# Optimization experiments

Measured on AMD Instinct MI355X. Metric: run time of the kernel, lower is better.

## Reference

```python
import jax, jax.numpy as jnp
import numpy as np

NUM_HEADS = 12
NEG_INF = -1e30  # stand-in for -inf; exp underflows to 0 identically, avoids nan in grads


def setup_inputs() -> dict:
    key = jax.random.key(0)
    ks = jax.random.split(key, 8)
    B, H, W, EXTRA, C = 8, 32, 32, 64, 768
    N = H * W + EXTRA  # 1088 image tokens + task tokens
    hd = C // NUM_HEADS  # 64
    s = 0.02
    x = jax.random.normal(ks[0], (B, N, C), dtype=jnp.float32)
    qkv_w = jax.random.normal(ks[1], (3 * C, C), dtype=jnp.float32) * s
    qkv_b = jax.random.normal(ks[2], (3 * C,), dtype=jnp.float32) * s
    proj_w = jax.random.normal(ks[3], (C, C), dtype=jnp.float32) * s
    proj_b = jax.random.normal(ks[4], (C,), dtype=jnp.float32) * s
    rel_pos_h = jax.random.normal(ks[5], (2 * H - 1, hd), dtype=jnp.float32) * s
    rel_pos_w = jax.random.normal(ks[6], (2 * W - 1, hd), dtype=jnp.float32) * s
    # mask the trailing 32 key tokens per batch element (rows keep valid keys)
    key_padding_mask = jnp.broadcast_to(jnp.arange(N)[None, :] >= N - 32, (B, N))
    return {"x": x, "qkv_w": qkv_w, "qkv_b": qkv_b, "proj_w": proj_w,
            "proj_b": proj_b, "rel_pos_h": rel_pos_h, "rel_pos_w": rel_pos_w,
            "key_padding_mask": key_padding_mask, "H": H, "W": W}


def _get_rel_pos(q_size, k_size, rel_pos):
    # q_size == k_size and rel_pos.shape[0] == 2*q_size-1 here -> no interpolation branch
    coords = jnp.arange(q_size)[:, None] - jnp.arange(k_size)[None, :] + (k_size - 1)
    return rel_pos[coords]  # (q_size, k_size, head_dim)


def reference(x, qkv_w, qkv_b, proj_w, proj_b, rel_pos_h, rel_pos_w,
              key_padding_mask, H, W):
    B, N, C = x.shape
    nh = NUM_HEADS
    hd = C // nh
    scale = hd ** -0.5
    HW = H * W
    # qkv projection -> (3, B*nh, N, hd)
    qkv = (x @ qkv_w.T + qkv_b).reshape(B, N, 3, nh, hd)
    qkv = jnp.transpose(qkv, (2, 0, 3, 1, 4)).reshape(3, B * nh, N, hd)
    q, k, v = qkv[0], qkv[1], qkv[2]
    attn = jnp.einsum('bqd,bkd->bqk', q * scale, k)  # (B*nh, N, N)
    # decomposed relative position bias on the HxW grid block
    Rh = _get_rel_pos(H, H, rel_pos_h)  # (H, H, hd)
    Rw = _get_rel_pos(W, W, rel_pos_w)  # (W, W, hd)
    r_q = q[:, :HW].reshape(B * nh, H, W, hd)
    rel_h = jnp.einsum('bhwc,hkc->bhwk', r_q, Rh)  # (B*nh, H, W, H)
    rel_w = jnp.einsum('bhwc,wkc->bhwk', r_q, Rw)  # (B*nh, H, W, W)
    bias = (rel_h[:, :, :, :, None] + rel_w[:, :, :, None, :]).reshape(B * nh, HW, HW)
    attn = attn.at[:, :HW, :HW].add(bias)
    # key padding mask fusion: (B, N) -> (B*nh, 1, N), broadcast over queries
    mask = jnp.broadcast_to(key_padding_mask[:, None, None, :], (B, nh, 1, N))
    mask = mask.reshape(B * nh, 1, N)
    attn = jnp.where(mask, NEG_INF, attn)
    attn = jax.nn.softmax(attn, axis=-1)
    out = jnp.einsum('bqk,bkd->bqd', attn, v).reshape(B, nh, N, hd)
    out = jnp.transpose(out, (0, 2, 1, 3)).reshape(B, N, C)
    return out @ proj_w.T + proj_b
```

## Files before the change

### kernel.cpp

```cpp
#include <hip/hip_runtime.h>
#include <stdint.h>


typedef __attribute__((ext_vector_type(8))) short bf16x8;
typedef __attribute__((ext_vector_type(4))) float f32x4;
typedef __attribute__((ext_vector_type(16))) float f32x16;
typedef __attribute__((ext_vector_type(2))) int i32x2;
typedef __attribute__((ext_vector_type(4))) int i32x4;

#define DEVINL static __device__ __forceinline__

DEVINL unsigned short f2bf(float f) {
  unsigned u = __builtin_bit_cast(unsigned, f);
  u += 0x7FFFu + ((u >> 16) & 1u);
  return (unsigned short)(u >> 16);
}
DEVINL float bf2f(unsigned short h) {
  unsigned u = ((unsigned)h) << 16;
  return __builtin_bit_cast(float, u);
}
DEVINL void gload_lds16(const void* g, void* l) {
  __builtin_amdgcn_global_load_lds(
      (const __attribute__((address_space(1))) unsigned int*)g,
      (__attribute__((address_space(3))) unsigned int*)l, 16, 0, 0);
}
DEVINL float exp2_hw(float x) {
  float r;
  asm("v_exp_f32 %0, %1" : "=v"(r) : "v"(x));
  return r;
}
DEVINL unsigned cvtpk_bf16(float lo, float hi) {
  unsigned r;
  asm("v_cvt_pk_bf16_f32 %0, %1, %2" : "=v"(r) : "v"(lo), "v"(hi));
  return r;
}

__global__ void k_cvt(const float* __restrict__ in, unsigned short* __restrict__ out, int n4) {
  int i = blockIdx.x * 256 + threadIdx.x;
  int stride = gridDim.x * 256;
  for (; i < n4; i += stride) {
    float4 v = ((const float4*)in)[i];
    ushort4 o = make_ushort4(f2bf(v.x), f2bf(v.y), f2bf(v.z), f2bf(v.w));
    ((ushort4*)out)[i] = o;
  }
}

__global__ void k_cvt2(const float* __restrict__ a, const float* __restrict__ b,
                       unsigned short* __restrict__ oa, unsigned short* __restrict__ ob,
                       int n4each) {
  int i = blockIdx.x * 256 + threadIdx.x;
  if (i < n4each) {
    float4 v = ((const float4*)a)[i];
    ((ushort4*)oa)[i] = make_ushort4(f2bf(v.x), f2bf(v.y), f2bf(v.z), f2bf(v.w));
  } else if (i < 2 * n4each) {
    int j = i - n4each;
    float4 v = ((const float4*)b)[j];
    ((ushort4*)ob)[j] = make_ushort4(f2bf(v.x), f2bf(v.y), f2bf(v.z), f2bf(v.w));
  }
}

template <int EPI, int NT, int JPX>
__global__ __launch_bounds__(256) void k_gemm_bt(
    const unsigned short* __restrict__ A, const unsigned short* __restrict__ Bm,
    const float* __restrict__ bias, float* __restrict__ Cf,
    unsigned short* __restrict__ oq, unsigned short* __restrict__ ok,
    unsigned short* __restrict__ ov, int M, int N, int K) {
  __shared__ __align__(16) unsigned short lA[128 * 64];
  __shared__ __align__(16) unsigned short lB[128 * 64];
  const int f = blockIdx.y * gridDim.x + blockIdx.x;
  const int job = (f & 7) * JPX + (f >> 3);
  const int xt = job / NT, yt = job - xt * NT;
  const int t = threadIdx.x;
  const int w = t >> 6, l = t & 63;
  const int wm = w >> 1, wn = w & 1;
  const int g = l >> 4, li = l & 15;
  const int row0 = xt * 128, col0 = yt * 128;
  const unsigned short* Ab = A + (size_t)row0 * K;
  const unsigned short* Bb = Bm + (size_t)col0 * K;
  const f32x4 zero = {0.f, 0.f, 0.f, 0.f};
  f32x4 acc[4][4];
#pragma unroll
  for (int i = 0; i < 4; ++i)
#pragma unroll
    for (int j = 0; j < 4; ++j) acc[i][j] = zero;

  const int srow = t >> 3;
  const int scs = (t & 7) ^ (srow & 7);

  for (int kt = 0; kt < K; kt += 64) {
#pragma unroll
    for (int p = 0; p < 4; ++p) {
      int r = p * 32 + srow;
      gload_lds16(Ab + (size_t)r * K + kt + scs * 8, lA + p * 2048 + w * 512);
      gload_lds16(Bb + (size_t)r * K + kt + scs * 8, lB + p * 2048 + w * 512);
    }
    __syncthreads();
#pragma unroll
    for (int kh = 0; kh < 2; ++kh) {
      bf16x8 af[4], bfv[4];
#pragma unroll
      for (int mf = 0; mf < 4; ++mf) {
        int r = wm * 64 + mf * 16 + li;
        int c8 = (kh * 4 + g) ^ (r & 7);
        af[mf] = *(const bf16x8*)(lA + r * 64 + c8 * 8);
      }
#pragma unroll
      for (int nf = 0; nf < 4; ++nf) {
        int r = wn * 64 + nf * 16 + li;
        int c8 = (kh * 4 + g) ^ (r & 7);
        bfv[nf] = *(const bf16x8*)(lB + r * 64 + c8 * 8);
      }
#pragma unroll
      for (int mf = 0; mf < 4; ++mf)
#pragma unroll
        for (int nf = 0; nf < 4; ++nf)
          acc[mf][nf] = __builtin_amdgcn_mfma_f32_16x16x32_bf16(af[mf], bfv[nf], acc[mf][nf], 0, 0, 0);
    }
    __syncthreads();
  }

#pragma unroll
  for (int mf = 0; mf < 4; ++mf) {
#pragma unroll
    for (int nf = 0; nf < 4; ++nf) {
      const int jc = col0 + wn * 64 + nf * 16 + li;
      const float bj = bias[jc];
#pragma unroll
      for (int rg = 0; rg < 4; ++rg) {
        const int m = row0 + wm * 64 + mf * 16 + g * 4 + rg;
        float val = acc[mf][nf][rg] + bj;
        if (EPI == 0) {
          int which = jc / 768;
          int jr = jc - which * 768;
          int head = jr >> 6, d = jr & 63;
          int b = m / 1088;
          int n = m - b * 1088;
          size_t idx = (((size_t)(b * 12 + head)) * 1088 + n) * 64 + d;
          if (which == 0) val *= 0.18033688011112042f;
          unsigned short bv = f2bf(val);
          if (which == 0) oq[idx] = bv;
          else if (which == 1) ok[idx] = bv;
          else ov[idx] = bv;
        } else {
          Cf[(size_t)m * N + jc] = val;
        }
      }
    }
  }
}

__global__ __launch_bounds__(256) void k_vt(const unsigned short* __restrict__ v,
                                            unsigned short* __restrict__ vt) {
  __shared__ unsigned short tile[64 * 66];
  const int bh = blockIdx.y, nt = blockIdx.x, t = threadIdx.x;
  const unsigned short* src = v + (((size_t)bh * 1088) + nt * 64) * 64;
#pragma unroll
  for (int i = 0; i < 2; ++i) {
    int c = t + 256 * i;
    int r = c >> 3, d8 = (c & 7) * 8;
    uint4 val = *(const uint4*)(src + (size_t)r * 64 + d8);
    const unsigned short* s8 = (const unsigned short*)&val;
#pragma unroll
    for (int j = 0; j < 8; ++j) tile[r * 66 + d8 + j] = s8[j];
  }
  __syncthreads();
  unsigned short* dst = vt + ((size_t)bh * 64) * 1088 + nt * 64;
#pragma unroll
  for (int i = 0; i < 2; ++i) {
    int c = t + 256 * i;
    int d = c >> 3, n8 = (c & 7) * 8;
    unsigned short tmp[8];
#pragma unroll
    for (int j = 0; j < 8; ++j) tmp[j] = tile[(n8 + j) * 66 + d];
    *(uint4*)(dst + (size_t)d * 1088 + n8) = *(const uint4*)tmp;
  }
}

__global__ __launch_bounds__(256) void k_relpos(const unsigned short* __restrict__ qbf,
                                                const unsigned short* __restrict__ rphbf,
                                                const unsigned short* __restrict__ rpwbf,
                                                float* __restrict__ relhT,
                                                float* __restrict__ relw) {
  __shared__ float gw[4][32 * 64];
  const int bh = blockIdx.y, t = threadIdx.x;
  const int wv = t >> 6, l = t & 63;
  const int h = blockIdx.x * 4 + wv;
  const int lk = l & 31, hf = l >> 5;

  bf16x8 qf[4];
  {
    const unsigned short* qp = qbf + (((size_t)bh * 1088) + h * 32 + lk) * 64 + hf * 8;
#pragma unroll
    for (int db = 0; db < 4; ++db) qf[db] = *(const bf16x8*)(qp + db * 16);
  }

  f32x16 dh, g0, g1;
#pragma unroll
  for (int i = 0; i < 16; ++i) { dh[i] = 0.f; g0[i] = 0.f; g1[i] = 0.f; }

  {
    const unsigned short* bp = rphbf + (size_t)(h + 31 - lk) * 64 + hf * 8;
#pragma unroll
    for (int db = 0; db < 4; ++db) {
      bf16x8 bfr = *(const bf16x8*)(bp + db * 16);
      dh = __builtin_amdgcn_mfma_f32_32x32x16_bf16(qf[db], bfr, dh, 0, 0, 0);
    }
  }
  {
    const unsigned short* bp0 = rpwbf + (size_t)lk * 64 + hf * 8;
    const unsigned short* bp1 = rpwbf + (size_t)(32 + lk) * 64 + hf * 8;
#pragma unroll
    for (int db = 0; db < 4; ++db) {
      bf16x8 b0 = *(const bf16x8*)(bp0 + db * 16);
      bf16x8 b1 = *(const bf16x8*)(bp1 + db * 16);
      g0 = __builtin_amdgcn_mfma_f32_32x32x16_bf16(qf[db], b0, g0, 0, 0, 0);
      g1 = __builtin_amdgcn_mfma_f32_32x32x16_bf16(qf[db], b1, g1, 0, 0, 0);
    }
  }
  float* G = gw[wv];
#pragma unroll
  for (int i = 0; i < 16; ++i) {
    int row = (i & 3) + 8 * (i >> 2) + 4 * hf;
    G[row * 64 + lk] = g0[i];
    G[row * 64 + 32 + lk] = g1[i];
  }
  f32x16 dwv;
#pragma unroll
  for (int i = 0; i < 16; ++i) {
    int row = (i & 3) + 8 * (i >> 2) + 4 * hf;
    dwv[i] = G[row * 65 + 31 - lk];
  }
  asm volatile("s_waitcnt lgkmcnt(0)" ::: "memory");
#pragma unroll
  for (int i = 0; i < 16; ++i) {
    int row = (i & 3) + 8 * (i >> 2) + 4 * hf;
    G[row * 33 + lk] = dh[i];
  }
  float dhT[16];
#pragma unroll
  for (int i = 0; i < 16; ++i) {
    int row = (i & 3) + 8 * (i >> 2) + 4 * hf;
    dhT[i] = G[lk * 33 + row];
  }
  float* outw = relw + (((size_t)bh * 1024) + h * 32) * 32;
  float* outhT = relhT + (size_t)bh * 32 * 1024;
#pragma unroll
  for (int i = 0; i < 16; ++i) {
    int row = (i & 3) + 8 * (i >> 2) + 4 * hf;
    outw[row * 32 + lk] = dwv[i] * 8.0f;
    outhT[(size_t)row * 1024 + h * 32 + lk] = dhT[i] * 8.0f;
  }
}

__global__ __launch_bounds__(256) void k_flash(
    const unsigned short* __restrict__ qbf, const unsigned short* __restrict__ kbf,
    const unsigned short* __restrict__ vtbf, const float* __restrict__ relhT,
    const float* __restrict__ relw, unsigned short* __restrict__ attnbf) {
  __shared__ __align__(16) char smem[32768];
  unsigned short* lK0 = (unsigned short*)smem;
  unsigned short* lV0 = (unsigned short*)(smem + 8192);
  unsigned short* lK1 = (unsigned short*)(smem + 16384);
  unsigned short* lV1 = (unsigned short*)(smem + 24576);

  const int f = blockIdx.y * 9 + blockIdx.x;
  const int ii = f >> 3;
  const int bh = (f & 7) * 12 + ii / 9;
  const int qt = ii % 9;
  const int t = threadIdx.x;
  const int w = t >> 6, l = t & 63;
  const int lq = l & 31;
  const int hf = l >> 5;
  const int q_in_blk = w * 32 + lq;
  const int qglob = qt * 128 + q_in_blk;
  const bool hasbias = (qt < 8);
  const bool qvalid = (qglob < 1088);
  const int row1 = 32 + lq;

  const unsigned short* Kb = kbf + (size_t)bh * 1088 * 64;
  const unsigned short* Vb = vtbf + (size_t)bh * 64 * 1088;
  const float* rhTb = relhT + (size_t)bh * 32 * 1024;
  const int srow = t >> 3;
  const int scs = (t & 7) ^ (srow & 7);

  auto stage = [&](int kc, unsigned short* dK, unsigned short* dV) {
#pragma unroll
    for (int p = 0; p < 2; ++p) {
      int r = p * 32 + srow;
      gload_lds16(Kb + ((size_t)(kc * 64 + r)) * 64 + scs * 8, dK + p * 2048 + w * 512);
      gload_lds16(Vb + (size_t)r * 1088 + kc * 64 + scs * 8, dV + p * 2048 + w * 512);
    }
  };

  stage(0, lK0, lV0);

  float rw[16];
#pragma unroll
  for (int i = 0; i < 16; ++i) rw[i] = 0.f;
  float rhc0 = 0.f, rhc1 = 0.f;
  if (hasbias) {
    const float* rwp = relw + (((size_t)bh * 1024) + qglob) * 32;
#pragma unroll
    for (int i = 0; i < 16; ++i) {
      int kw = (i & 3) + 8 * (i >> 2) + 4 * hf;
      rw[i] = rwp[kw];
    }
    rhc0 = rhTb[qglob];
    rhc1 = rhTb[1024 + qglob];
  }
  bf16x8 qf[4];
  {
    const unsigned short* qp = qbf + (((size_t)bh * 1088) + qglob) * 64 + hf * 8;
#pragma unroll
    for (int d = 0; d < 4; ++d) qf[d] = *(const bf16x8*)(qp + d * 16);
  }

  f32x16 o0, o1;
#pragma unroll
  for (int i = 0; i < 16; ++i) { o0[i] = 0.f; o1[i] = 0.f; }
  float mrun = -1e30f, lrun = 0.f;

  asm volatile("s_waitcnt vmcnt(0) lgkmcnt(0)" ::: "memory");
  __builtin_amdgcn_s_barrier();

  auto body = [&](int kc, unsigned short* cK, unsigned short* cV,
                  unsigned short* nK, unsigned short* nV) {
    stage(kc + 1, nK, nV);
    float rhn0 = 0.f, rhn1 = 0.f;
    if (hasbias && kc < 15) {
      rhn0 = rhTb[(2 * kc + 2) * 1024 + qglob];
      rhn1 = rhTb[(2 * kc + 3) * 1024 + qglob];
    }
    f32x16 s0, s1;
#pragma unroll
    for (int i = 0; i < 16; ++i) { s0[i] = rhc0 + rw[i]; s1[i] = rhc1 + rw[i]; }
    __builtin_amdgcn_s_setprio(1);
#pragma unroll
    for (int db = 0; db < 4; ++db) {
      int sl = db * 2 + hf;
      bf16x8 k0 = *(const bf16x8*)(cK + lq * 64 + ((sl ^ (lq & 7)) << 3));
      bf16x8 k1 = *(const bf16x8*)(cK + row1 * 64 + ((sl ^ (row1 & 7)) << 3));
      s0 = __builtin_amdgcn_mfma_f32_32x32x16_bf16(k0, qf[db], s0, 0, 0, 0);
      s1 = __builtin_amdgcn_mfma_f32_32x32x16_bf16(k1, qf[db], s1, 0, 0, 0);
    }
    __builtin_amdgcn_s_setprio(0);
    float p[32];
#pragma unroll
    for (int i = 0; i < 16; ++i) p[i] = s0[i];
#pragma unroll
    for (int i = 0; i < 16; ++i) p[16 + i] = s1[i];
    float mt[16];
#pragma unroll
    for (int i = 0; i < 16; ++i) mt[i] = fmaxf(p[i], p[16 + i]);
#pragma unroll
    for (int s = 8; s > 0; s >>= 1)
#pragma unroll
      for (int i = 0; i < s; ++i) mt[i] = fmaxf(mt[i], mt[i + s]);
    float mc = fmaxf(mt[0], __shfl_xor(mt[0], 32));
    if (!__all(mc - mrun <= 8.0f)) {
      float mnew = fmaxf(mrun, mc);
      float al = exp2_hw(mrun - mnew);
      lrun *= al;
#pragma unroll
      for (int i = 0; i < 16; ++i) { o0[i] *= al; o1[i] *= al; }
      mrun = mnew;
    }
#pragma unroll
    for (int i = 0; i < 32; ++i) p[i] = exp2_hw(p[i] - mrun);
    float st[16];
#pragma unroll
    for (int i = 0; i < 16; ++i) st[i] = p[i] + p[16 + i];
#pragma unroll
    for (int s = 8; s > 0; s >>= 1)
#pragma unroll
      for (int i = 0; i < s; ++i) st[i] += st[i + s];
    lrun += st[0] + __shfl_xor(st[0], 32);
#pragma unroll
    for (int kb = 0; kb < 4; ++kb) {
      unsigned X0 = cvtpk_bf16(p[kb * 8 + 0], p[kb * 8 + 1]);
      unsigned X1 = cvtpk_bf16(p[kb * 8 + 2], p[kb * 8 + 3]);
      unsigned Y0 = cvtpk_bf16(p[kb * 8 + 4], p[kb * 8 + 5]);
      unsigned Y1 = cvtpk_bf16(p[kb * 8 + 6], p[kb * 8 + 7]);
      i32x2 r0 = __builtin_amdgcn_permlane32_swap(X0, Y0, false, false);
      i32x2 r1 = __builtin_amdgcn_permlane32_swap(X1, Y1, false, false);
      i32x4 pd;
      pd.x = r0.x; pd.y = r1.x; pd.z = r0.y; pd.w = r1.y;
      bf16x8 pf = __builtin_bit_cast(bf16x8, pd);
      int sl = kb * 2 + hf;
      bf16x8 v0 = *(const bf16x8*)(cV + lq * 64 + ((sl ^ (lq & 7)) << 3));
      bf16x8 v1 = *(const bf16x8*)(cV + row1 * 64 + ((sl ^ (row1 & 7)) << 3));
      __builtin_amdgcn_s_setprio(1);
      o0 = __builtin_amdgcn_mfma_f32_32x32x16_bf16(v0, pf, o0, 0, 0, 0);
      o1 = __builtin_amdgcn_mfma_f32_32x32x16_bf16(v1, pf, o1, 0, 0, 0);
      __builtin_amdgcn_s_setprio(0);
    }
    rhc0 = rhn0; rhc1 = rhn1;
    asm volatile("s_waitcnt vmcnt(0)" ::: "memory");
    __builtin_amdgcn_s_barrier();
  };

  for (int it = 0; it < 8; ++it) {
    body(2 * it, lK0, lV0, lK1, lV1);
    body(2 * it + 1, lK1, lV1, lK0, lV0);
  }

  {
    f32x16 s0;
#pragma unroll
    for (int i = 0; i < 16; ++i) s0[i] = 0.f;
    __builtin_amdgcn_s_setprio(1);
#pragma unroll
    for (int db = 0; db < 4; ++db) {
      int sl = db * 2 + hf;
      bf16x8 k0 = *(const bf16x8*)(lK0 + lq * 64 + ((sl ^ (lq & 7)) << 3));
      s0 = __builtin_amdgcn_mfma_f32_32x32x16_bf16(k0, qf[db], s0, 0, 0, 0);
    }
    __builtin_amdgcn_s_setprio(0);
    float p[16];
#pragma unroll
    for (int i = 0; i < 16; ++i) p[i] = s0[i];
    float mt[8];
#pragma unroll
    for (int i = 0; i < 8; ++i) mt[i] = fmaxf(p[i], p[8 + i]);
#pragma unroll
    for (int s = 4; s > 0; s >>= 1)
#pragma unroll
      for (int i = 0; i < s; ++i) mt[i] = fmaxf(mt[i], mt[i + s]);
    float mc = fmaxf(mt[0], __shfl_xor(mt[0], 32));
    if (!__all(mc - mrun <= 8.0f)) {
      float mnew = fmaxf(mrun, mc);
      float al = exp2_hw(mrun - mnew);
      lrun *= al;
#pragma unroll
      for (int i = 0; i < 16; ++i) { o0[i] *= al; o1[i] *= al; }
      mrun = mnew;
    }
#pragma unroll
    for (int i = 0; i < 16; ++i) p[i] = exp2_hw(p[i] - mrun);
    float st[8];
#pragma unroll
    for (int i = 0; i < 8; ++i) st[i] = p[i] + p[8 + i];
#pragma unroll
    for (int s = 4; s > 0; s >>= 1)
#pragma unroll
      for (int i = 0; i < s; ++i) st[i] += st[i + s];
    lrun += st[0] + __shfl_xor(st[0], 32);
#pragma unroll
    for (int kb = 0; kb < 2; ++kb) {
      unsigned X0 = cvtpk_bf16(p[kb * 8 + 0], p[kb * 8 + 1]);
      unsigned X1 = cvtpk_bf16(p[kb * 8 + 2], p[kb * 8 + 3]);
      unsigned Y0 = cvtpk_bf16(p[kb * 8 + 4], p[kb * 8 + 5]);
      unsigned Y1 = cvtpk_bf16(p[kb * 8 + 6], p[kb * 8 + 7]);
      i32x2 r0 = __builtin_amdgcn_permlane32_swap(X0, Y0, false, false);
      i32x2 r1 = __builtin_amdgcn_permlane32_swap(X1, Y1, false, false);
      i32x4 pd;
      pd.x = r0.x; pd.y = r1.x; pd.z = r0.y; pd.w = r1.y;
      bf16x8 pf = __builtin_bit_cast(bf16x8, pd);
      int sl = kb * 2 + hf;
      bf16x8 v0 = *(const bf16x8*)(lV0 + lq * 64 + ((sl ^ (lq & 7)) << 3));
      bf16x8 v1 = *(const bf16x8*)(lV0 + row1 * 64 + ((sl ^ (row1 & 7)) << 3));
      __builtin_amdgcn_s_setprio(1);
      o0 = __builtin_amdgcn_mfma_f32_32x32x16_bf16(v0, pf, o0, 0, 0, 0);
      o1 = __builtin_amdgcn_mfma_f32_32x32x16_bf16(v1, pf, o1, 0, 0, 0);
      __builtin_amdgcn_s_setprio(0);
    }
    __builtin_amdgcn_s_barrier();
  }

  float* tile = (float*)(smem + w * 8192);
  float inv = 1.f / lrun;
#pragma unroll
  for (int i = 0; i < 16; ++i) {
    int d0 = (i & 3) + 8 * (i >> 2) + 4 * hf;
    tile[d0 * 32 + (lq ^ (d0 & 31))] = o0[i] * inv;
    int d1 = 32 + d0;
    tile[d1 * 32 + (lq ^ (d1 & 31))] = o1[i] * inv;
  }
  asm volatile("s_waitcnt lgkmcnt(0)" ::: "memory");
  if (qvalid) {
    const int b = bh / 12, head = bh - (bh / 12) * 12;
    unsigned dw[16];
#pragma unroll
    for (int j = 0; j < 16; ++j) {
      int da = hf * 32 + 2 * j, dbi = da + 1;
      float v0 = tile[da * 32 + (lq ^ (da & 31))];
      float v1 = tile[dbi * 32 + (lq ^ (dbi & 31))];
      dw[j] = cvtpk_bf16(v0, v1);
    }
    unsigned short* dst = attnbf + (((size_t)b * 1088) + qglob) * 768 + head * 64 + hf * 32;
#pragma unroll
    for (int j = 0; j < 4; ++j) {
      uint4 u = make_uint4(dw[4 * j], dw[4 * j + 1], dw[4 * j + 2], dw[4 * j + 3]);
      *(uint4*)(dst + j * 8) = u;
    }
  }
}

extern "C" void kernel_launch(void* const* d_in, const int* in_sizes, int n_in,
                              void* d_out, int out_size, void* d_ws, size_t ws_size,
                              hipStream_t stream) {
  const float* x = (const float*)d_in[0];
  const float* qkv_w = (const float*)d_in[1];
  const float* qkv_b = (const float*)d_in[2];
  const float* proj_w = (const float*)d_in[3];
  const float* proj_b = (const float*)d_in[4];
  const float* rph = (const float*)d_in[5];
  const float* rpw = (const float*)d_in[6];
  float* out = (float*)d_out;

  char* ws = (char*)d_ws;
  unsigned short* xbf = (unsigned short*)(ws + 0);
  unsigned short* attnbf = xbf;
  unsigned short* wqkv = (unsigned short*)(ws + 13369344);
  unsigned short* wproj = (unsigned short*)(ws + 16908288);
  unsigned short* qbf = (unsigned short*)(ws + 18087936);
  unsigned short* kbf = (unsigned short*)(ws + 31457280);
  unsigned short* vbf = (unsigned short*)(ws + 44826624);
  unsigned short* vtbf = (unsigned short*)(ws + 58195968);
  float* relhT = (float*)(ws + 71565312);
  float* relw = (float*)(ws + 84148224);
  unsigned short* rphbf = (unsigned short*)(ws + 44826624);
  unsigned short* rpwbf = (unsigned short*)(ws + 44826624 + 8192);

  k_cvt<<<dim3(1024), dim3(256), 0, stream>>>(x, xbf, 8704 * 768 / 4);
  k_cvt<<<dim3(512), dim3(256), 0, stream>>>(qkv_w, wqkv, 2304 * 768 / 4);
  k_cvt<<<dim3(128), dim3(256), 0, stream>>>(proj_w, wproj, 768 * 768 / 4);
  k_gemm_bt<0, 18, 153><<<dim3(68, 18), dim3(256), 0, stream>>>(
      xbf, wqkv, qkv_b, nullptr, qbf, kbf, vbf, 8704, 2304, 768);
  k_vt<<<dim3(17, 96), dim3(256), 0, stream>>>(vbf, vtbf);
  k_cvt2<<<dim3(8), dim3(256), 0, stream>>>(rph, rpw, rphbf, rpwbf, 63 * 64 / 4);
  k_relpos<<<dim3(8, 96), dim3(256), 0, stream>>>(qbf, rphbf, rpwbf, relhT, relw);
  k_flash<<<dim3(9, 96), dim3(256), 0, stream>>>(qbf, kbf, vtbf, relhT, relw, attnbf);
  k_gemm_bt<1, 6, 51><<<dim3(68, 6), dim3(256), 0, stream>>>(
      attnbf, wproj, proj_b, out, nullptr, nullptr, nullptr, 8704, 768, 768);
}
```

Baseline: 172.3 us.

## Double flash query tile to 256 rows with 512 threads; fuse fp32-to-bf16 conversions

The flash attention kernel now runs 8 waves per block covering 256 query rows, so each staged K/V tile is shared by twice as many queries. The grid drops from 9 to 5 query tiles per head, and the last tile clamps its out-of-range Q loads. The epilogue writes through shared memory in two passes because the 32KB buffer only fits four waves' output tiles. Separately, the three input conversion launches are merged into one kernel. The trade-offs are more padded work in the final tile (1280 vs 1088 rows), fewer blocks to spread across the CUs, and extra block-wide barriers.

Measured after the change: 165.1 us. 1.04x faster.

```diff
diff --git a/kernel.cpp b/kernel.cpp
--- a/kernel.cpp
+++ b/kernel.cpp
@@ -35,13 +35,23 @@
   return r;
 }
 
-__global__ void k_cvt(const float* __restrict__ in, unsigned short* __restrict__ out, int n4) {
+__global__ void k_cvt_all(const float* __restrict__ x, const float* __restrict__ qkv_w,
+                          const float* __restrict__ proj_w,
+                          unsigned short* __restrict__ xbf, unsigned short* __restrict__ wqkv,
+                          unsigned short* __restrict__ wproj) {
+  const int NX = 8704 * 768 / 4, NQ = 2304 * 768 / 4, NP = 768 * 768 / 4;
+  const int total = NX + NQ + NP;
   int i = blockIdx.x * 256 + threadIdx.x;
-  int stride = gridDim.x * 256;
-  for (; i < n4; i += stride) {
-    float4 v = ((const float4*)in)[i];
-    ushort4 o = make_ushort4(f2bf(v.x), f2bf(v.y), f2bf(v.z), f2bf(v.w));
-    ((ushort4*)out)[i] = o;
+  const int stride = gridDim.x * 256;
+  for (; i < total; i += stride) {
+    const float* src;
+    unsigned short* dst;
+    int j = i;
+    if (j < NX) { src = x; dst = xbf; }
+    else if ((j -= NX) < NQ) { src = qkv_w; dst = wqkv; }
+    else { j -= NQ; src = proj_w; dst = wproj; }
+    float4 v = ((const float4*)src)[j];
+    ((ushort4*)dst)[j] = make_ushort4(f2bf(v.x), f2bf(v.y), f2bf(v.z), f2bf(v.w));
   }
 }
 
@@ -252,7 +262,7 @@
   }
 }
 
-__global__ __launch_bounds__(256) void k_flash(
+__global__ __launch_bounds__(512) void k_flash(
     const unsigned short* __restrict__ qbf, const unsigned short* __restrict__ kbf,
     const unsigned short* __restrict__ vtbf, const float* __restrict__ relhT,
     const float* __restrict__ relw, unsigned short* __restrict__ attnbf) {
@@ -262,17 +272,17 @@
   unsigned short* lK1 = (unsigned short*)(smem + 16384);
   unsigned short* lV1 = (unsigned short*)(smem + 24576);
 
-  const int f = blockIdx.y * 9 + blockIdx.x;
+  const int f = blockIdx.y * 5 + blockIdx.x;
   const int ii = f >> 3;
-  const int bh = (f & 7) * 12 + ii / 9;
-  const int qt = ii % 9;
+  const int bh = (f & 7) * 12 + ii / 5;
+  const int qt = ii % 5;
   const int t = threadIdx.x;
   const int w = t >> 6, l = t & 63;
   const int lq = l & 31;
   const int hf = l >> 5;
   const int q_in_blk = w * 32 + lq;
-  const int qglob = qt * 128 + q_in_blk;
-  const bool hasbias = (qt < 8);
+  const int qglob = qt * 256 + q_in_blk;
+  const bool hasbias = (qglob < 1024);
   const bool qvalid = (qglob < 1088);
   const int row1 = 32 + lq;
 
@@ -283,12 +293,8 @@
   const int scs = (t & 7) ^ (srow & 7);
 
   auto stage = [&](int kc, unsigned short* dK, unsigned short* dV) {
-#pragma unroll
-    for (int p = 0; p < 2; ++p) {
-      int r = p * 32 + srow;
-      gload_lds16(Kb + ((size_t)(kc * 64 + r)) * 64 + scs * 8, dK + p * 2048 + w * 512);
-      gload_lds16(Vb + (size_t)r * 1088 + kc * 64 + scs * 8, dV + p * 2048 + w * 512);
-    }
+    gload_lds16(Kb + ((size_t)(kc * 64 + srow)) * 64 + scs * 8, dK + t * 8);
+    gload_lds16(Vb + (size_t)srow * 1088 + kc * 64 + scs * 8, dV + t * 8);
   };
 
   stage(0, lK0, lV0);
@@ -309,7 +315,8 @@
   }
   bf16x8 qf[4];
   {
-    const unsigned short* qp = qbf + (((size_t)bh * 1088) + qglob) * 64 + hf * 8;
+    const int qldr = qvalid ? qglob : 1087;
+    const unsigned short* qp = qbf + (((size_t)bh * 1088) + qldr) * 64 + hf * 8;
 #pragma unroll
     for (int d = 0; d < 4; ++d) qf[d] = *(const bf16x8*)(qp + d * 16);
   }
@@ -463,35 +470,42 @@
       o1 = __builtin_amdgcn_mfma_f32_32x32x16_bf16(v1, pf, o1, 0, 0, 0);
       __builtin_amdgcn_s_setprio(0);
     }
-    __builtin_amdgcn_s_barrier();
-  }
-
-  float* tile = (float*)(smem + w * 8192);
-  float inv = 1.f / lrun;
-#pragma unroll
-  for (int i = 0; i < 16; ++i) {
-    int d0 = (i & 3) + 8 * (i >> 2) + 4 * hf;
-    tile[d0 * 32 + (lq ^ (d0 & 31))] = o0[i] * inv;
-    int d1 = 32 + d0;
-    tile[d1 * 32 + (lq ^ (d1 & 31))] = o1[i] * inv;
-  }
-  asm volatile("s_waitcnt lgkmcnt(0)" ::: "memory");
-  if (qvalid) {
-    const int b = bh / 12, head = bh - (bh / 12) * 12;
-    unsigned dw[16];
-#pragma unroll
-    for (int j = 0; j < 16; ++j) {
-      int da = hf * 32 + 2 * j, dbi = da + 1;
-      float v0 = tile[da * 32 + (lq ^ (da & 31))];
-      float v1 = tile[dbi * 32 + (lq ^ (dbi & 31))];
-      dw[j] = cvtpk_bf16(v0, v1);
-    }
-    unsigned short* dst = attnbf + (((size_t)b * 1088) + qglob) * 768 + head * 64 + hf * 32;
-#pragma unroll
-    for (int j = 0; j < 4; ++j) {
-      uint4 u = make_uint4(dw[4 * j], dw[4 * j + 1], dw[4 * j + 2], dw[4 * j + 3]);
-      *(uint4*)(dst + j * 8) = u;
-    }
+  }
+  __syncthreads();
+
+  const float inv = 1.f / lrun;
+  float* tile = (float*)(smem + (size_t)(w & 3) * 8192);
+  const int grp = w >> 2;
+  const int b = bh / 12, head = bh - (bh / 12) * 12;
+  unsigned short* dst = attnbf + (((size_t)b * 1088) + qglob) * 768 + head * 64 + hf * 32;
+#pragma unroll
+  for (int pass = 0; pass < 2; ++pass) {
+    if (grp == pass) {
+#pragma unroll
+      for (int i = 0; i < 16; ++i) {
+        int d0 = (i & 3) + 8 * (i >> 2) + 4 * hf;
+        tile[d0 * 32 + (lq ^ (d0 & 31))] = o0[i] * inv;
+        int d1 = 32 + d0;
+        tile[d1 * 32 + (lq ^ (d1 & 31))] = o1[i] * inv;
+      }
+    }
+    __syncthreads();
+    if (grp == pass && qvalid) {
+      unsigned dw[16];
+#pragma unroll
+      for (int j = 0; j < 16; ++j) {
+        int da = hf * 32 + 2 * j, dbi = da + 1;
+        float v0 = tile[da * 32 + (lq ^ (da & 31))];
+        float v1 = tile[dbi * 32 + (lq ^ (dbi & 31))];
+        dw[j] = cvtpk_bf16(v0, v1);
+      }
+#pragma unroll
+      for (int j = 0; j < 4; ++j) {
+        uint4 u = make_uint4(dw[4 * j], dw[4 * j + 1], dw[4 * j + 2], dw[4 * j + 3]);
+        *(uint4*)(dst + j * 8) = u;
+      }
+    }
+    __syncthreads();
   }
 }
 
@@ -521,15 +535,13 @@
   unsigned short* rphbf = (unsigned short*)(ws + 44826624);
   unsigned short* rpwbf = (unsigned short*)(ws + 44826624 + 8192);
 
-  k_cvt<<<dim3(1024), dim3(256), 0, stream>>>(x, xbf, 8704 * 768 / 4);
-  k_cvt<<<dim3(512), dim3(256), 0, stream>>>(qkv_w, wqkv, 2304 * 768 / 4);
-  k_cvt<<<dim3(128), dim3(256), 0, stream>>>(proj_w, wproj, 768 * 768 / 4);
+  k_cvt_all<<<dim3(2048), dim3(256), 0, stream>>>(x, qkv_w, proj_w, xbf, wqkv, wproj);
   k_gemm_bt<0, 18, 153><<<dim3(68, 18), dim3(256), 0, stream>>>(
       xbf, wqkv, qkv_b, nullptr, qbf, kbf, vbf, 8704, 2304, 768);
   k_vt<<<dim3(17, 96), dim3(256), 0, stream>>>(vbf, vtbf);
   k_cvt2<<<dim3(8), dim3(256), 0, stream>>>(rph, rpw, rphbf, rpwbf, 63 * 64 / 4);
   k_relpos<<<dim3(8, 96), dim3(256), 0, stream>>>(qbf, rphbf, rpwbf, relhT, relw);
-  k_flash<<<dim3(9, 96), dim3(256), 0, stream>>>(qbf, kbf, vtbf, relhT, relw, attnbf);
+  k_flash<<<dim3(5, 96), dim3(512), 0, stream>>>(qbf, kbf, vtbf, relhT, relw, attnbf);
   k_gemm_bt<1, 6, 51><<<dim3(68, 6), dim3(256), 0, stream>>>(
       attnbf, wproj, proj_b, out, nullptr, nullptr, nullptr, 8704, 768, 768);
 }
```
